# Kernel tuning notes

Measured on AMD Instinct MI355X. Metric: run time of the kernel, lower is better.

The kernel has to match this reference:

```python
import jax, jax.numpy as jnp
import numpy as np

FEAT_STRIDE = 16
PRE_NMS = 6000
POST_NMS = 300
NMS_THRESH = 0.7
NEG_THR = 0.3
POS_THR = 0.7
RPN_BATCH = 256
FG_FRAC = 0.5
SCALES = (8, 16, 32)
RATIOS = (0.5, 1.0, 2.0)
A = len(SCALES) * len(RATIOS)  # 9


def _generate_anchors():
    base = 16.0
    ctr = (base - 1.0) * 0.5
    size = base * base
    out = []
    for r in RATIOS:
        ws = np.round(np.sqrt(size / r))
        hs = np.round(ws * r)
        for s in SCALES:
            W = ws * s
            H = hs * s
            out.append([ctr - 0.5 * (W - 1), ctr - 0.5 * (H - 1),
                        ctr + 0.5 * (W - 1), ctr + 0.5 * (H - 1)])
    return np.array(out, np.float32)  # [9,4]


def _conv(x, w, b, pad):
    y = jax.lax.conv_general_dilated(x, w, (1, 1), [(pad, pad), (pad, pad)],
                                     dimension_numbers=('NCHW', 'OIHW', 'NCHW'))
    return y + b[None, :, None, None]


def _all_anchors(H, W):
    base = jnp.asarray(_generate_anchors())
    sx = jnp.arange(W, dtype=jnp.float32) * FEAT_STRIDE
    sy = jnp.arange(H, dtype=jnp.float32) * FEAT_STRIDE
    gy, gx = jnp.meshgrid(sy, sx, indexing='ij')
    shifts = jnp.stack([gx, gy, gx, gy], -1).reshape(-1, 1, 4)  # [H*W,1,4]
    return (shifts + base[None]).reshape(-1, 4)  # (h,w,a) order, [H*W*A,4]


def _decode(anchors, deltas):
    w = anchors[:, 2] - anchors[:, 0] + 1.0
    h = anchors[:, 3] - anchors[:, 1] + 1.0
    cx = anchors[:, 0] + 0.5 * w
    cy = anchors[:, 1] + 0.5 * h
    pcx = deltas[:, 0] * w + cx
    pcy = deltas[:, 1] * h + cy
    pw = jnp.exp(deltas[:, 2]) * w
    ph = jnp.exp(deltas[:, 3]) * h
    return jnp.stack([pcx - 0.5 * pw, pcy - 0.5 * ph, pcx + 0.5 * pw, pcy + 0.5 * ph], -1)


def _encode(anchors, gt):
    ew = anchors[:, 2] - anchors[:, 0] + 1.0
    eh = anchors[:, 3] - anchors[:, 1] + 1.0
    ecx = anchors[:, 0] + 0.5 * ew
    ecy = anchors[:, 1] + 0.5 * eh
    gw = gt[:, 2] - gt[:, 0] + 1.0
    gh = gt[:, 3] - gt[:, 1] + 1.0
    gcx = gt[:, 0] + 0.5 * gw
    gcy = gt[:, 1] + 0.5 * gh
    return jnp.stack([(gcx - ecx) / ew, (gcy - ecy) / eh,
                      jnp.log(gw / ew), jnp.log(gh / eh)], -1)


def _nms(boxes, scores, thresh, max_out):
    x1, y1, x2, y2 = boxes[:, 0], boxes[:, 1], boxes[:, 2], boxes[:, 3]
    areas = (x2 - x1 + 1.0) * (y2 - y1 + 1.0)
    N = boxes.shape[0]

    def body(k, st):
        valid, sel, selv = st
        s = jnp.where(valid, scores, -jnp.inf)
        i = jnp.argmax(s)
        ok = s[i] > -jnp.inf
        iw = jnp.maximum(jnp.minimum(x2[i], x2) - jnp.maximum(x1[i], x1) + 1.0, 0.0)
        ih = jnp.maximum(jnp.minimum(y2[i], y2) - jnp.maximum(y1[i], y1) + 1.0, 0.0)
        inter = iw * ih
        iou = inter / (areas[i] + areas - inter)
        valid = valid & (iou <= thresh)
        return valid, sel.at[k].set(i.astype(jnp.int32)), selv.at[k].set(ok)

    st = jax.lax.fori_loop(0, max_out, body,
                           (jnp.ones(N, bool), jnp.zeros(max_out, jnp.int32), jnp.zeros(max_out, bool)))
    return st[1], st[2]


def _propose_one(scores, deltas, anchors, imh, imw):
    boxes = _decode(anchors, deltas)
    boxes = jnp.stack([jnp.clip(boxes[:, 0], 0.0, imw - 1.0),
                       jnp.clip(boxes[:, 1], 0.0, imh - 1.0),
                       jnp.clip(boxes[:, 2], 0.0, imw - 1.0),
                       jnp.clip(boxes[:, 3], 0.0, imh - 1.0)], -1)
    top_s, idx = jax.lax.top_k(scores, PRE_NMS)
    top_b = boxes[idx]
    sel, selv = _nms(top_b, top_s, NMS_THRESH, POST_NMS)
    return top_b[sel] * selv[:, None].astype(top_b.dtype)  # [POST_NMS,4], zero rows when exhausted


def _anchor_target_one(gt, imh, imw, rfg, rbg, anchors):
    N = anchors.shape[0]
    ax1, ay1, ax2, ay2 = anchors[:, 0], anchors[:, 1], anchors[:, 2], anchors[:, 3]
    inside = (ax1 >= 0) & (ay1 >= 0) & (ax2 < imw) & (ay2 < imh)
    gx1, gy1, gx2, gy2 = gt[:, 0], gt[:, 1], gt[:, 2], gt[:, 3]
    gw = gx2 - gx1 + 1.0
    gh = gy2 - gy1 + 1.0
    gt_valid = ~((gw == 1.0) & (gh == 1.0))  # all-zero padded gt boxes
    aw = ax2 - ax1 + 1.0
    ah = ay2 - ay1 + 1.0
    iw = jnp.maximum(jnp.minimum(ax2[:, None], gx2[None, :]) - jnp.maximum(ax1[:, None], gx1[None, :]) + 1.0, 0.0)
    ih = jnp.maximum(jnp.minimum(ay2[:, None], gy2[None, :]) - jnp.maximum(ay1[:, None], gy1[None, :]) + 1.0, 0.0)
    inter = iw * ih
    iou = inter / ((aw * ah)[:, None] + (gw * gh)[None, :] - inter)  # [N,K]
    iou = jnp.where(gt_valid[None, :], iou, 0.0)
    iou = jnp.where(inside[:, None], iou, -1.0)  # outside anchors excluded, as in original
    max_ov = iou.max(1)
    arg = iou.argmax(1)
    gt_max = iou.max(0)
    gt_max = jnp.where(gt_max <= 0.0, 1e-5, gt_max)
    keep = (iou == gt_max[None, :]).any(1)  # anchors with max overlap per gt -> fg
    labels = jnp.full(N, -1.0, jnp.float32)
    labels = jnp.where(max_ov < NEG_THR, 0.0, labels)
    labels = jnp.where(keep, 1.0, labels)
    labels = jnp.where(max_ov >= POS_THR, 1.0, labels)
    labels = jnp.where(inside, labels, -1.0)

    def ranks(r, mask):
        order = jnp.argsort(jnp.where(mask, r, 2.0))
        return jnp.zeros(N, jnp.int32).at[order].set(jnp.arange(N, dtype=jnp.int32))

    num_fg = int(FG_FRAC * RPN_BATCH)
    fg_keep = (labels == 1.0) & (ranks(rfg, labels == 1.0) < num_fg)
    num_bg = RPN_BATCH - fg_keep.sum()
    bg_keep = (labels == 0.0) & (ranks(rbg, labels == 0.0) < num_bg)
    labels = jnp.where(fg_keep, 1.0, jnp.where(bg_keep, 0.0, -1.0))
    targets = _encode(anchors, gt[arg, :4])
    ones4 = jnp.ones((1, 4), jnp.float32)
    in_w = (labels == 1.0).astype(jnp.float32)[:, None] * ones4
    n_ex = (labels >= 0).sum().astype(jnp.float32)
    out_w = jnp.where(labels >= 0, 1.0 / n_ex, 0.0)[:, None] * ones4
    return labels, targets, in_w, out_w


def _rpn_forward(base_feat, im_info, gt_boxes, conv_w, conv_b, cls_w, cls_b, bbox_w, bbox_b):
    B, _, H, W = base_feat.shape
    x = jax.nn.relu(_conv(base_feat, conv_w, conv_b, 1))
    cls_score = _conv(x, cls_w, cls_b, 0)                 # [B,2A,H,W]
    # reshape(x,2) -> softmax over axis 1 -> reshape back
    prob = jax.nn.softmax(cls_score.reshape(B, 2, A * H, W), axis=1).reshape(B, 2 * A, H, W)
    bbox_pred = _conv(x, bbox_w, bbox_b, 0)               # [B,4A,H,W]
    anchors = _all_anchors(H, W)                          # [H*W*A,4]

    # ---- proposal layer (detached in original) ----
    fg = prob[:, A:, :, :].transpose(0, 2, 3, 1).reshape(B, -1)        # (h,w,a)
    deltas = bbox_pred.transpose(0, 2, 3, 1).reshape(B, -1, 4)
    rois_boxes = jax.vmap(_propose_one, in_axes=(0, 0, None, 0, 0))(
        jax.lax.stop_gradient(fg), jax.lax.stop_gradient(deltas), anchors, im_info[:, 0], im_info[:, 1])
    batch_idx = jnp.broadcast_to(jnp.arange(B, dtype=rois_boxes.dtype)[:, None, None], (B, POST_NMS, 1))
    rois = jnp.concatenate([batch_idx, rois_boxes], -1)   # [B,POST_NMS,5]

    # ---- anchor target layer (training path) ----
    key = jax.random.key(42)
    rfg = jax.random.uniform(key, (B, anchors.shape[0]))
    rbg = jax.random.uniform(jax.random.fold_in(key, 1), (B, anchors.shape[0]))
    labels, targets, in_w, out_w = jax.vmap(_anchor_target_one, in_axes=(0, 0, 0, 0, 0, None))(
        gt_boxes, im_info[:, 0], im_info[:, 1], rfg, rbg, anchors)
    # rearrange (h,w,a) -> (a,h,w) layouts to match torch permutes
    labels = labels.reshape(B, H, W, A).transpose(0, 3, 1, 2).reshape(B, -1)
    targets = targets.reshape(B, H, W, A * 4).transpose(0, 3, 1, 2)
    in_w = in_w.reshape(B, H, W, A * 4).transpose(0, 3, 1, 2)
    out_w = out_w.reshape(B, H, W, A * 4).transpose(0, 3, 1, 2)

    # cross-entropy over kept anchors
    logits = cls_score.reshape(B, 2, A, H, W).transpose(0, 2, 3, 4, 1).reshape(-1, 2)
    lab = labels.reshape(-1)
    m = (lab >= 0).astype(logits.dtype)
    logp = jax.nn.log_softmax(logits, axis=-1)
    idx = jnp.clip(lab, 0.0, 1.0).astype(jnp.int32)
    nll = -jnp.take_along_axis(logp, idx[:, None], axis=1)[:, 0]
    loss_cls = (nll * m).sum() / m.sum()

    # smooth-L1 box loss, sigma=3, sum dims [1,2,3] then mean over batch
    sigma2 = 9.0
    diff = in_w * (bbox_pred - targets)
    ad = jnp.abs(diff)
    flag = (ad < 1.0 / sigma2).astype(diff.dtype)
    lb = flag * 0.5 * sigma2 * diff * diff + (1.0 - flag) * (ad - 0.5 / sigma2)
    loss_box = (out_w * lb).sum(axis=(1, 2, 3)).mean()
    return rois, loss_cls, loss_box


def setup_inputs() -> dict:
    key = jax.random.key(0)
    ks = jax.random.split(key, 9)
    B, C, H, W = 4, 512, 50, 76
    base_feat = jax.random.normal(ks[0], (B, C, H, W), jnp.float32)
    conv_w = jax.random.normal(ks[1], (512, C, 3, 3), jnp.float32) * 0.01
    conv_b = jnp.zeros((512,), jnp.float32)
    cls_w = jax.random.normal(ks[2], (18, 512, 1, 1), jnp.float32) * 0.01
    cls_b = jnp.zeros((18,), jnp.float32)
    bbox_w = jax.random.normal(ks[3], (36, 512, 1, 1), jnp.float32) * 0.01
    bbox_b = jnp.zeros((36,), jnp.float32)
    imh, imw = float(H * FEAT_STRIDE), float(W * FEAT_STRIDE)
    im_info = jnp.tile(jnp.array([imh, imw, 1.0], jnp.float32), (B, 1))
    K = 20
    cx = jax.random.uniform(ks[4], (B, K)) * (imw - 100.0) + 50.0
    cy = jax.random.uniform(ks[5], (B, K)) * (imh - 100.0) + 50.0
    bw = jax.random.uniform(ks[6], (B, K)) * 270.0 + 30.0
    bh = jax.random.uniform(ks[7], (B, K)) * 270.0 + 30.0
    x1 = jnp.clip(cx - 0.5 * bw, 0.0, imw - 1.0)
    x2 = jnp.clip(cx + 0.5 * bw, 0.0, imw - 1.0)
    y1 = jnp.clip(cy - 0.5 * bh, 0.0, imh - 1.0)
    y2 = jnp.clip(cy + 0.5 * bh, 0.0, imh - 1.0)
    cls = jax.random.randint(ks[8], (B, K), 1, 21).astype(jnp.float32)
    gt_boxes = jnp.stack([x1, y1, x2, y2, cls], -1)
    num_boxes = jnp.full((B,), K, jnp.int32)
    return {"base_feat": base_feat, "im_info": im_info, "gt_boxes": gt_boxes,
            "num_boxes": num_boxes, "conv_w": conv_w, "conv_b": conv_b,
            "cls_w": cls_w, "cls_b": cls_b, "bbox_w": bbox_w, "bbox_b": bbox_b}


def reference(base_feat, im_info, gt_boxes, num_boxes, conv_w, conv_b, cls_w, cls_b, bbox_w, bbox_b):
    # num_boxes is implicitly handled via zero-padded gt_boxes (as in the original layer)
    return _rpn_forward(base_feat, im_info, gt_boxes, conv_w, conv_b, cls_w, cls_b, bbox_w, bbox_b)
```

## Files before the change

kernel.cpp:

```cpp
#include <hip/hip_runtime.h>
#include <stdint.h>

#define HHH 50
#define WWW 76
#define NPIX 3800
#define NA 34200
#define PRE 6000
#define POST 300
#define NW 94
#define CIN 512
#define COUT 512
#define NBATCH 4
#define NGT 20
#define TFHALF 68400u
#define XTB 2252800

typedef __bf16 bf16x8 __attribute__((ext_vector_type(8)));
typedef float f32x4 __attribute__((ext_vector_type(4)));
typedef unsigned int u32x4v __attribute__((ext_vector_type(4)));

__device__ static inline f32x4 MFMA16(bf16x8 a, bf16x8 b, f32x4 c) {
  return __builtin_amdgcn_mfma_f32_16x16x32_bf16(a, b, c, 0, 0, 0);
}
__device__ static inline bf16x8 LD8(const unsigned short* p) {
  return __builtin_bit_cast(bf16x8, *(const u32x4v*)p);
}

__host__ __device__ static inline void tf2x32(unsigned k0, unsigned k1, unsigned& x0, unsigned& x1) {
  unsigned k2 = k0 ^ k1 ^ 0x1BD11BDAu;
#define TFR(r) do { x0 += x1; x1 = (x1 << (r)) | (x1 >> (32 - (r))); x1 ^= x0; } while (0)
  x0 += k0; x1 += k1;
  TFR(13); TFR(15); TFR(26); TFR(6);
  x0 += k1; x1 += k2 + 1u;
  TFR(17); TFR(29); TFR(16); TFR(24);
  x0 += k2; x1 += k0 + 2u;
  TFR(13); TFR(15); TFR(26); TFR(6);
  x0 += k0; x1 += k1 + 3u;
  TFR(17); TFR(29); TFR(16); TFR(24);
  x0 += k1; x1 += k2 + 4u;
  TFR(13); TFR(15); TFR(26); TFR(6);
  x0 += k2; x1 += k0 + 5u;
#undef TFR
}

__device__ static inline unsigned tf_u23(unsigned k0, unsigned k1, unsigned p) {
  unsigned x0, x1;
  if (p < TFHALF) { x0 = p; x1 = p + TFHALF; tf2x32(k0, k1, x0, x1); return x0 >> 9; }
  x0 = p - TFHALF; x1 = p; tf2x32(k0, k1, x0, x1); return x1 >> 9;
}

__device__ const float BA[9][4] = {
  {-84.f, -40.f,  99.f,  55.f}, {-176.f, -88.f, 191.f, 103.f}, {-360.f, -184.f, 375.f, 199.f},
  {-56.f, -56.f,  71.f,  71.f}, {-120.f, -120.f, 135.f, 135.f}, {-248.f, -248.f, 263.f, 263.f},
  {-36.f, -80.f,  51.f,  95.f}, {-80.f, -168.f,  95.f, 183.f}, {-168.f, -344.f, 183.f, 359.f}
};

__device__ static inline unsigned monoF(float f) {
  int b = __float_as_int(f);
  unsigned u = (unsigned)b;
  return (b < 0) ? ~u : (u | 0x80000000u);
}
__device__ static inline float unmonoF(unsigned u) {
  unsigned b = (u & 0x80000000u) ? (u ^ 0x80000000u) : ~u;
  return __int_as_float((int)b);
}

__device__ static inline void split3(float v, unsigned short& h, unsigned short& m, unsigned short& l) {
  __bf16 b0 = (__bf16)v;  float f0 = (float)b0;
  float r = v - f0;       __bf16 b1 = (__bf16)r;  float f1 = (float)b1;
  float r2 = r - f1;      __bf16 b2 = (__bf16)r2;
  h = __builtin_bit_cast(unsigned short, b0);
  m = __builtin_bit_cast(unsigned short, b1);
  l = __builtin_bit_cast(unsigned short, b2);
}

__global__ void k_split_x(const float* __restrict__ feat, unsigned short* __restrict__ x0,
                          unsigned short* __restrict__ x1, unsigned short* __restrict__ x2) {
  int tid = blockIdx.x * 256 + threadIdx.x;
  if (tid >= NBATCH * XTB) return;
  int b = tid / XTB;
  int rem = tid - b * XTB;
  int pg = rem >> 13;
  int r2 = rem & 8191;
  int cg = r2 >> 7;
  int po = (r2 >> 3) & 15;
  int cl = r2 & 7;
  int ci = cg * 8 + cl;
  int px = pg * 16 + po;
  int hq = px / 80, wq = px - hq * 80;
  float v = 0.f;
  if (hq >= 2 && hq < 52 && wq >= 1 && wq < 77)
    v = feat[((size_t)(b * 512 + ci)) * NPIX + (hq - 2) * 76 + (wq - 1)];
  unsigned short h, m, l;
  split3(v, h, m, l);
  x0[tid] = h; x1[tid] = m; x2[tid] = l;
}

__global__ void k_split_w(const float* __restrict__ cw, unsigned short* __restrict__ w0,
                          unsigned short* __restrict__ w1, unsigned short* __restrict__ w2,
                          unsigned* __restrict__ gtmaxU, int* __restrict__ cnts, float* __restrict__ accums) {
  int tid = blockIdx.x * 256 + threadIdx.x;
  if (blockIdx.x == 0) {
    int t = threadIdx.x;
    if (t < NBATCH * NGT) gtmaxU[t] = 0x407FFFFFu;
    if (t < 8) cnts[t] = 0;
    if (t < 8) accums[t] = 0.f;
  }
  if (tid >= 9 * 64 * 512 * 8) return;
  int cl = tid & 7;
  int co = (tid >> 3) & 511;
  int cg = (tid >> 12) & 63;
  int tap = tid >> 18;
  int ci = cg * 8 + cl;
  float v = cw[((size_t)co * 512 + ci) * 9 + tap];
  unsigned short h, m, l;
  split3(v, h, m, l);
  w0[tid] = h; w1[tid] = m; w2[tid] = l;
}

__global__ void k_tr_w1(const float* __restrict__ clsw, const float* __restrict__ bbw, float* __restrict__ wt1) {
  int tid = blockIdx.x * 256 + threadIdx.x;
  if (tid >= CIN * 64) return;
  int c = tid & 63, ci = tid >> 6;
  float v = 0.f;
  if (c < 18) v = clsw[c * 512 + ci];
  else if (c < 54) v = bbw[(c - 18) * 512 + ci];
  wt1[tid] = v;
}

__global__ __launch_bounds__(256, 2) void k_conv3(
    const unsigned short* __restrict__ XT0, const unsigned short* __restrict__ XT1,
    const unsigned short* __restrict__ XT2,
    const unsigned short* __restrict__ WT0, const unsigned short* __restrict__ WT1,
    const unsigned short* __restrict__ WT2,
    const float* __restrict__ bias, float* __restrict__ out) {
  const int d = blockIdx.x;
  const int copair = (d >> 1) & 3, half = d & 1, g = d >> 3;
  const int cob = copair * 2 + (g & 1);
  const int pxb = half * 64 + (g >> 1);
  const int pxp = pxb & 31, b = pxb >> 5;
  const int co0 = cob * 64;
  const int px0 = 160 + pxp * 128;
  const int t = threadIdx.x, l = t & 63, wv = t >> 6;
  const int wr = wv >> 1, wc = wv & 1;
  const int l15 = l & 15, lq = l >> 4;
  f32x4 cmain[2][4], ccorr[2][4];
  double accd[2][4][4];
#pragma unroll
  for (int c = 0; c < 2; ++c)
#pragma unroll
    for (int p = 0; p < 4; ++p) {
      cmain[c][p] = (f32x4)(0.f); ccorr[c][p] = (f32x4)(0.f);
#pragma unroll
      for (int r = 0; r < 4; ++r) accd[c][p][r] = 0.0;
    }
  const unsigned short* xt0 = XT0 + (size_t)b * XTB;
  const unsigned short* xt1 = XT1 + (size_t)b * XTB;
  const unsigned short* xt2 = XT2 + (size_t)b * XTB;
  const int coA = wr * 32 + l15;
  const int OFFT[9] = {-81, -80, -79, -1, 0, 1, 79, 80, 81};
  const int pxw = px0 + wc * 64 + l15;

  for (int kg = 0; kg < 16; ++kg) {
    const int cgl = kg * 4 + lq;
    const int cglo = cgl * 128;
    const size_t aro = ((size_t)cgl * 512 + co0 + coA) * 8;
#pragma unroll
    for (int tap = 0; tap < 9; ++tap) {
      const size_t ao = aro + (size_t)tap * (64 * 512 * 8);
      bf16x8 A0[2], A1[2], A2[2];
      A0[0] = LD8(WT0 + ao); A0[1] = LD8(WT0 + ao + 128);
      A1[0] = LD8(WT1 + ao); A1[1] = LD8(WT1 + ao + 128);
      A2[0] = LD8(WT2 + ao); A2[1] = LD8(WT2 + ao + 128);
      const int pxbase = pxw + OFFT[tap];
      const size_t eob = (size_t)((pxbase >> 4) * 8192 + (pxbase & 15) * 8 + cglo);
#pragma unroll
      for (int p = 0; p < 4; ++p) {
        const size_t eo = eob + (size_t)p * 8192;
        bf16x8 B0 = LD8(xt0 + eo);
        bf16x8 B1 = LD8(xt1 + eo);
        bf16x8 B2 = LD8(xt2 + eo);
#pragma unroll
        for (int c = 0; c < 2; ++c) {
          cmain[c][p] = MFMA16(A0[c], B0, cmain[c][p]);
          ccorr[c][p] = MFMA16(A2[c], B0, ccorr[c][p]);
          ccorr[c][p] = MFMA16(A0[c], B2, ccorr[c][p]);
          ccorr[c][p] = MFMA16(A1[c], B1, ccorr[c][p]);
          ccorr[c][p] = MFMA16(A1[c], B0, ccorr[c][p]);
          ccorr[c][p] = MFMA16(A0[c], B1, ccorr[c][p]);
        }
      }
    }
    if (kg & 1) {
#pragma unroll
      for (int c = 0; c < 2; ++c)
#pragma unroll
        for (int p = 0; p < 4; ++p) {
#pragma unroll
          for (int r = 0; r < 4; ++r) accd[c][p][r] += (double)cmain[c][p][r];
          cmain[c][p] = (f32x4)(0.f);
        }
    }
  }
  const size_t outb = ((size_t)b * 512 + co0) * NPIX;
#pragma unroll
  for (int c = 0; c < 2; ++c)
#pragma unroll
    for (int p = 0; p < 4; ++p)
#pragma unroll
      for (int r = 0; r < 4; ++r) {
        int coL = wr * 32 + c * 16 + lq * 4 + r;
        int px = px0 + wc * 64 + p * 16 + l15;
        int hq = px / 80, wq = px - hq * 80;
        if (hq >= 2 && hq < 52 && wq >= 1 && wq < 77) {
          float v = (float)(accd[c][p][r] + (double)ccorr[c][p][r]) + bias[co0 + coL];
          out[outb + (size_t)coL * NPIX + (hq - 2) * 76 + (wq - 1)] = fmaxf(v, 0.f);
        }
      }
}

__global__ __launch_bounds__(256) void k_conv1(const float* __restrict__ x, const float* __restrict__ wt1,
                                               const float* __restrict__ clsb, const float* __restrict__ bbb,
                                               float* __restrict__ clsS, float* __restrict__ bbp) {
  const int b = blockIdx.y;
  const int px0 = blockIdx.x * 128;
  const int t = threadIdx.x;
  const int cg = t & 7, pg = t >> 3;
  __shared__ float xs[16][128];
  __shared__ float ws[16][72];
  double acc[8][4];
#pragma unroll
  for (int i = 0; i < 8; ++i)
#pragma unroll
    for (int j = 0; j < 4; ++j) acc[i][j] = 0.0;
  const float* xb = x + (size_t)b * CIN * NPIX;
  for (int cc = 0; cc < CIN; cc += 16) {
#pragma unroll
    for (int e0 = 0; e0 < 8; ++e0) {
      int e = t + e0 * 256;
      int r = e >> 7, c = e & 127;
      int p = px0 + c;
      xs[r][c] = (p < NPIX) ? xb[(size_t)(cc + r) * NPIX + p] : 0.f;
    }
#pragma unroll
    for (int e0 = 0; e0 < 4; ++e0) {
      int e = t + e0 * 256;
      int r = e >> 6, c = e & 63;
      ws[r][c + ((c >> 5) << 2)] = wt1[(cc + r) * 64 + c];
    }
    __syncthreads();
    const int wcol = (cg << 3) + ((cg >> 2) << 2);
    const int xcol = pg << 2;
    float a32[8][4];
#pragma unroll
    for (int i = 0; i < 8; ++i)
#pragma unroll
      for (int j = 0; j < 4; ++j) a32[i][j] = 0.f;
#pragma unroll
    for (int k = 0; k < 16; ++k) {
      const float4 w0 = *(const float4*)&ws[k][wcol];
      const float4 w1 = *(const float4*)&ws[k][wcol + 4];
      const float4 xa = *(const float4*)&xs[k][xcol];
      const float wv[8] = {w0.x, w0.y, w0.z, w0.w, w1.x, w1.y, w1.z, w1.w};
      const float xv[4] = {xa.x, xa.y, xa.z, xa.w};
#pragma unroll
      for (int i = 0; i < 8; ++i)
#pragma unroll
        for (int j = 0; j < 4; ++j)
          a32[i][j] = fmaf(wv[i], xv[j], a32[i][j]);
    }
#pragma unroll
    for (int i = 0; i < 8; ++i)
#pragma unroll
      for (int j = 0; j < 4; ++j) acc[i][j] += (double)a32[i][j];
    __syncthreads();
  }
#pragma unroll
  for (int i = 0; i < 8; ++i) {
    int c = cg * 8 + i;
#pragma unroll
    for (int j = 0; j < 4; ++j) {
      int p = px0 + pg * 4 + j;
      if (p < NPIX) {
        if (c < 18) clsS[((size_t)b * 18 + c) * NPIX + p] = (float)acc[i][j] + clsb[c];
        else if (c < 54) bbp[((size_t)b * 36 + (c - 18)) * NPIX + p] = (float)acc[i][j] + bbb[c - 18];
      }
    }
  }
}

__global__ void k_decode(const float* __restrict__ clsS, const float* __restrict__ bbp,
                         const float* __restrict__ im_info, float* __restrict__ boxes,
                         unsigned long long* __restrict__ keys) {
  int tid = blockIdx.x * 256 + threadIdx.x;
  if (tid >= NBATCH * NA) return;
  int b = tid / NA, n = tid - b * NA;
  int a = n % 9, p = n / 9;
  int h = p / WWW, w = p - h * WWW;
  const float* cb = clsS + (size_t)b * 18 * NPIX;
  float s0 = cb[(size_t)a * NPIX + p];
  float s1 = cb[(size_t)(9 + a) * NPIX + p];
  float mx = fmaxf(s0, s1);
  float e0 = expf(s0 - mx), e1 = expf(s1 - mx);
  float fg = e1 / (e0 + e1);
  const float* bb = bbp + (size_t)b * 36 * NPIX;
  float d0 = bb[(size_t)(a * 4 + 0) * NPIX + p];
  float d1 = bb[(size_t)(a * 4 + 1) * NPIX + p];
  float d2 = bb[(size_t)(a * 4 + 2) * NPIX + p];
  float d3 = bb[(size_t)(a * 4 + 3) * NPIX + p];
  float ax1 = BA[a][0] + w * 16.f, ay1 = BA[a][1] + h * 16.f;
  float ax2 = BA[a][2] + w * 16.f, ay2 = BA[a][3] + h * 16.f;
  float aw = ax2 - ax1 + 1.f, ah = ay2 - ay1 + 1.f;
  float acx = ax1 + 0.5f * aw, acy = ay1 + 0.5f * ah;
  float pcx = d0 * aw + acx, pcy = d1 * ah + acy;
  float pw = expf(d2) * aw, ph = expf(d3) * ah;
  float imh = im_info[b * 3 + 0], imw = im_info[b * 3 + 1];
  float x1 = fminf(fmaxf(pcx - 0.5f * pw, 0.f), imw - 1.f);
  float y1 = fminf(fmaxf(pcy - 0.5f * ph, 0.f), imh - 1.f);
  float x2 = fminf(fmaxf(pcx + 0.5f * pw, 0.f), imw - 1.f);
  float y2 = fminf(fmaxf(pcy + 0.5f * ph, 0.f), imh - 1.f);
  float* bx = boxes + ((size_t)b * NA + n) * 4;
  bx[0] = x1; bx[1] = y1; bx[2] = x2; bx[3] = y2;
  unsigned fb = __float_as_uint(fg);
  keys[((size_t)b << 16) + n] = ((unsigned long long)fb << 32) | (unsigned)(~(unsigned)n);
}

__global__ __launch_bounds__(1024) void k_rsel_top(const unsigned long long* __restrict__ keys,
                                                   unsigned long long* __restrict__ comp) {
  const int b = blockIdx.x;
  const unsigned long long* kb = keys + ((size_t)b << 16);
  __shared__ int hist[16][256];
  __shared__ int histT[256];
  __shared__ unsigned long long sh_prefix;
  __shared__ unsigned sh_r;
  __shared__ int sh_cnt;
  const int t = threadIdx.x, wid = t >> 6, lane = t & 63;
  if (t == 0) { sh_prefix = 0ull; sh_r = PRE; sh_cnt = 0; }
  __syncthreads();
  for (int p = 5; p >= 0; --p) {
    for (int e = t; e < 4096; e += 1024) ((int*)hist)[e] = 0;
    __syncthreads();
    unsigned long long pref = sh_prefix;
    for (int i = t; i < NA; i += 1024) {
      unsigned long long k = kb[i];
      unsigned long long k48 = ((k >> 16) & 0xFFFFFFFF0000ull) | (k & 0xFFFFull);
      bool m = (p == 5) || ((k48 >> (8 * (p + 1))) == pref);
      if (m) atomicAdd(&hist[wid][(int)((k48 >> (8 * p)) & 255)], 1);
    }
    __syncthreads();
    if (t < 256) { int s = 0; for (int w = 0; w < 16; ++w) s += hist[w][t]; histT[t] = s; }
    __syncthreads();
    if (t == 0) {
      unsigned rr = sh_r; unsigned cum = 0;
      for (int v = 255; v >= 0; --v) {
        cum += (unsigned)histT[v];
        if (cum >= rr) { sh_r = rr - (cum - (unsigned)histT[v]); sh_prefix = (sh_prefix << 8) | (unsigned)v; break; }
      }
    }
    __syncthreads();
  }
  const unsigned long long thr48 = sh_prefix;
  for (int base = 0; base < NA; base += 1024) {
    int i = base + t;
    bool keep = false;
    unsigned long long k = 0ull;
    if (i < NA) {
      k = kb[i];
      unsigned long long k48 = ((k >> 16) & 0xFFFFFFFF0000ull) | (k & 0xFFFFull);
      keep = (k48 >= thr48);
    }
    unsigned long long bal = __ballot(keep);
    if (bal) {
      int leader = __ffsll(bal) - 1;
      int basepos = 0;
      if (lane == leader) basepos = atomicAdd(&sh_cnt, (int)__popcll(bal));
      basepos = __shfl(basepos, leader);
      if (keep) {
        int off = __popcll(bal & ((1ull << lane) - 1ull));
        comp[b * 8192 + basepos + off] = k;
      }
    }
  }
}

__global__ __launch_bounds__(1024) void k_sort_lds(const unsigned long long* __restrict__ comp,
                                                   const float* __restrict__ boxes,
                                                   float* __restrict__ tbx1, float* __restrict__ tby1,
                                                   float* __restrict__ tbx2, float* __restrict__ tby2,
                                                   float* __restrict__ tba) {
  __shared__ unsigned long long s[8192];
  const int b = blockIdx.x;
  const int t = threadIdx.x;
  const unsigned long long* cb = comp + b * 8192;
  for (int e = t; e < 8192; e += 1024) s[e] = (e < PRE) ? cb[e] : 0ull;
  __syncthreads();
  for (int k = 2; k <= 8192; k <<= 1) {
    for (int j = k >> 1; j >= 1; j >>= 1) {
      for (int q = t; q < 4096; q += 1024) {
        int i = ((q & ~(j - 1)) << 1) | (q & (j - 1));
        int pp = i | j;
        bool up = (i & k) == 0;
        unsigned long long a = s[i], d = s[pp];
        if (up ? (a < d) : (a > d)) { s[i] = d; s[pp] = a; }
      }
      __syncthreads();
    }
  }
  for (int e = t; e < PRE; e += 1024) {
    unsigned long long key = s[e];
    unsigned n = ~(unsigned)(key & 0xFFFFFFFFu);
    const float* bx = boxes + ((size_t)b * NA + n) * 4;
    float x1 = bx[0], y1 = bx[1], x2 = bx[2], y2 = bx[3];
    int o = b * PRE + e;
    tbx1[o] = x1; tby1[o] = y1; tbx2[o] = x2; tby2[o] = y2;
    tba[o] = (x2 - x1 + 1.f) * (y2 - y1 + 1.f);
  }
}

__global__ __launch_bounds__(256) void k_mask(const float* __restrict__ tbx1, const float* __restrict__ tby1,
                                              const float* __restrict__ tbx2, const float* __restrict__ tby2,
                                              const float* __restrict__ tba, unsigned long long* __restrict__ mask) {
  const int b = blockIdx.y;
  const int i0 = blockIdx.x * 64;
  const int t = threadIdx.x;
  __shared__ float jx1[2048], jy1[2048], jx2[2048], jy2[2048], ja[2048];
  __shared__ float ix1[64], iy1[64], ix2[64], iy2[64], ia[64];
  const float* bx1 = tbx1 + b * PRE;
  const float* by1 = tby1 + b * PRE;
  const float* bx2 = tbx2 + b * PRE;
  const float* by2 = tby2 + b * PRE;
  const float* ba2 = tba + b * PRE;
  if (t < 64) {
    int i = i0 + t;
    if (i < PRE) { ix1[t] = bx1[i]; iy1[t] = by1[i]; ix2[t] = bx2[i]; iy2[t] = by2[i]; ia[t] = ba2[i]; }
    else { ix1[t] = 0; iy1[t] = 0; ix2[t] = 0; iy2[t] = 0; ia[t] = 1; }
  }
  for (int c = 0; c < 3; ++c) {
    int j0 = c * 2048;
    for (int e = t; e < 2048; e += 256) {
      int j = j0 + e;
      if (j < PRE) { jx1[e] = bx1[j]; jy1[e] = by1[j]; jx2[e] = bx2[j]; jy2[e] = by2[j]; ja[e] = ba2[j]; }
      else { jx1[e] = 0; jy1[e] = 0; jx2[e] = 0; jy2[e] = 0; ja[e] = 1; }
    }
    __syncthreads();
    for (int task = t; task < 64 * 32; task += 256) {
      int il = task & 63, wl = task >> 6;
      int i = i0 + il;
      int wg = (j0 >> 6) + wl;
      if (i >= PRE || wg >= NW) continue;
      unsigned long long word = 0ull;
      float X1 = ix1[il], Y1 = iy1[il], X2 = ix2[il], Y2 = iy2[il], A = ia[il];
      for (int l = 0; l < 64; ++l) {
        int j = wg * 64 + l;
        if (j > i && j < PRE) {
          int e = j - j0;
          float iw = fminf(X2, jx2[e]) - fmaxf(X1, jx1[e]) + 1.f;
          float ih = fminf(Y2, jy2[e]) - fmaxf(Y1, jy1[e]) + 1.f;
          if (iw > 0.f && ih > 0.f) {
            float inter = iw * ih;
            float iou = inter / (A + ja[e] - inter);
            if (iou > 0.7f) word |= (1ull << l);
          }
        }
      }
      mask[((size_t)(b * PRE + i)) * NW + wg] = word;
    }
    __syncthreads();
  }
}

__global__ void k_nms(const unsigned long long* __restrict__ mask,
                      const float* __restrict__ tbx1, const float* __restrict__ tby1,
                      const float* __restrict__ tbx2, const float* __restrict__ tby2,
                      float* __restrict__ out) {
  const int b = blockIdx.x;
  const int lane = threadIdx.x;
  unsigned long long rem0 = 0ull;
  unsigned long long rem1;
  if (64 + lane < NW) rem1 = (64 + lane == NW - 1) ? ~((1ull << (PRE - (NW - 1) * 64)) - 1ull) : 0ull;
  else rem1 = ~0ull;
  int sc = 0;
  for (; sc < POST; ++sc) {
    unsigned long long a0 = ~rem0, a1 = ~rem1;
    unsigned long long bal0 = __ballot(a0 != 0ull);
    int w, l;
    if (bal0) {
      int src = __ffsll(bal0) - 1;
      unsigned long long av = __shfl(a0, src);
      w = src; l = __ffsll(av) - 1;
    } else {
      unsigned long long bal1 = __ballot(a1 != 0ull);
      if (!bal1) break;
      int src = __ffsll(bal1) - 1;
      unsigned long long av = __shfl(a1, src);
      w = 64 + src; l = __ffsll(av) - 1;
    }
    int j = w * 64 + l;
    if (lane < 5) {
      float v;
      if (lane == 0) v = (float)b;
      else if (lane == 1) v = tbx1[b * PRE + j];
      else if (lane == 2) v = tby1[b * PRE + j];
      else if (lane == 3) v = tbx2[b * PRE + j];
      else v = tby2[b * PRE + j];
      out[((size_t)(b * POST + sc)) * 5 + lane] = v;
    }
    const unsigned long long* row = mask + ((size_t)(b * PRE + j)) * NW;
    rem0 |= row[lane];
    if (64 + lane < NW) rem1 |= row[64 + lane];
    if (w < 64) { if (lane == w) rem0 |= (1ull << l); }
    else if (lane == w - 64) rem1 |= (1ull << l);
  }
  for (int r2 = sc; r2 < POST; ++r2)
    if (lane < 5) out[((size_t)(b * POST + r2)) * 5 + lane] = (lane == 0) ? (float)b : 0.f;
}

__global__ __launch_bounds__(256) void k_iouA(const float* __restrict__ gt_boxes, const float* __restrict__ im_info,
                                              float* __restrict__ iou, float* __restrict__ maxov,
                                              int* __restrict__ argm, unsigned* __restrict__ gtmaxU) {
  const int b = blockIdx.y;
  const int n = blockIdx.x * 256 + threadIdx.x;
  const int t = threadIdx.x, lane = t & 63, wv = t >> 6;
  __shared__ float g[NGT][6];
  __shared__ float wmax[4][NGT];
  if (t < NGT) {
    const float* gg = gt_boxes + (b * NGT + t) * 5;
    float x1 = gg[0], y1 = gg[1], x2 = gg[2], y2 = gg[3];
    g[t][0] = x1; g[t][1] = y1; g[t][2] = x2; g[t][3] = y2;
    float gw = x2 - x1 + 1.f, gh = y2 - y1 + 1.f;
    g[t][4] = gw * gh;
    g[t][5] = ((gw == 1.f) && (gh == 1.f)) ? 0.f : 1.f;
  }
  __syncthreads();
  const bool act = (n < NA);
  float vj[NGT];
  float best = -2.f;
  int barg = 0;
  if (act) {
    int a = n % 9, p = n / 9;
    int h = p / WWW, w = p - h * WWW;
    float ax1 = BA[a][0] + w * 16.f, ay1 = BA[a][1] + h * 16.f;
    float ax2 = BA[a][2] + w * 16.f, ay2 = BA[a][3] + h * 16.f;
    float imh = im_info[b * 3 + 0], imw = im_info[b * 3 + 1];
    bool inside = (ax1 >= 0.f) && (ay1 >= 0.f) && (ax2 < imw) && (ay2 < imh);
    float aw = ax2 - ax1 + 1.f, ah = ay2 - ay1 + 1.f;
    float aa = aw * ah;
    float* row = iou + ((size_t)(b * NA) + n) * NGT;
#pragma unroll
    for (int j = 0; j < NGT; ++j) {
      float iw = fmaxf(fminf(ax2, g[j][2]) - fmaxf(ax1, g[j][0]) + 1.f, 0.f);
      float ih = fmaxf(fminf(ay2, g[j][3]) - fmaxf(ay1, g[j][1]) + 1.f, 0.f);
      float inter = iw * ih;
      float v = inter / (aa + g[j][4] - inter);
      if (g[j][5] == 0.f) v = 0.f;
      if (!inside) v = -1.f;
      row[j] = v;
      vj[j] = v;
      if (v > best) { best = v; barg = j; }
    }
    maxov[b * NA + n] = best;
    argm[b * NA + n] = barg;
  } else {
#pragma unroll
    for (int j = 0; j < NGT; ++j) vj[j] = -1.f;
  }
#pragma unroll
  for (int j = 0; j < NGT; ++j) {
    float red = vj[j];
    for (int o = 32; o > 0; o >>= 1) red = fmaxf(red, __shfl_xor(red, o));
    if (lane == 0) wmax[wv][j] = red;
  }
  __syncthreads();
  if (t < NGT) {
    float m = fmaxf(fmaxf(wmax[0][t], wmax[1][t]), fmaxf(wmax[2][t], wmax[3][t]));
    if (m > 0.f) atomicMax(&gtmaxU[b * NGT + t], monoF(m));
  }
}

__global__ __launch_bounds__(256) void k_labels(const float* __restrict__ iou, const float* __restrict__ maxov,
                                                const unsigned* __restrict__ gtmaxU, const float* __restrict__ im_info,
                                                unsigned kf0, unsigned kf1, unsigned kb0, unsigned kb1,
                                                int* __restrict__ labels, unsigned* __restrict__ ufg,
                                                unsigned* __restrict__ ubg, int* __restrict__ cnts) {
  const int b = blockIdx.y;
  const int n = blockIdx.x * 256 + threadIdx.x;
  __shared__ float gmf[NGT];
  if (threadIdx.x < NGT) {
    float gm = unmonoF(gtmaxU[b * NGT + threadIdx.x]);
    gmf[threadIdx.x] = (gm <= 0.f) ? 1e-5f : gm;
  }
  __syncthreads();
  int label = -1;
  if (n < NA) {
    int a = n % 9, p = n / 9;
    int h = p / WWW, w = p - h * WWW;
    float ax1 = BA[a][0] + w * 16.f, ay1 = BA[a][1] + h * 16.f;
    float ax2 = BA[a][2] + w * 16.f, ay2 = BA[a][3] + h * 16.f;
    float imh = im_info[b * 3 + 0], imw = im_info[b * 3 + 1];
    bool inside = (ax1 >= 0.f) && (ay1 >= 0.f) && (ax2 < imw) && (ay2 < imh);
    float mo = maxov[b * NA + n];
    const float* row = iou + ((size_t)(b * NA) + n) * NGT;
    bool keep = false;
#pragma unroll
    for (int j = 0; j < NGT; ++j) keep = keep || (row[j] == gmf[j]);
    if (mo < 0.3f) label = 0;
    if (keep) label = 1;
    if (mo >= 0.7f) label = 1;
    if (!inside) label = -1;
    labels[b * NA + n] = label;
    unsigned pp = (unsigned)(b * NA + n);
    ufg[b * NA + n] = (label == 1) ? tf_u23(kf0, kf1, pp) : 0x00FFFFFFu;
    ubg[b * NA + n] = (label == 0) ? tf_u23(kb0, kb1, pp) : 0x00FFFFFFu;
  }
  unsigned long long bf = __ballot(label == 1);
  unsigned long long bb = __ballot(label == 0);
  if ((threadIdx.x & 63) == 0) {
    atomicAdd(&cnts[b], (int)__popcll(bf));
    atomicAdd(&cnts[4 + b], (int)__popcll(bb));
  }
}

__global__ __launch_bounds__(1024) void k_rsel_samp(const unsigned* __restrict__ ufg, const unsigned* __restrict__ ubg,
                                                    const int* __restrict__ cnts, unsigned* __restrict__ selp,
                                                    float* __restrict__ nexf) {
  const int blk = blockIdx.x;
  const int b = blk >> 1, cls = blk & 1;
  const unsigned* u = (cls == 0 ? ufg : ubg) + (size_t)b * NA;
  const int fcnt = cnts[b], bcnt = cnts[4 + b];
  const int kk = (cls == 0) ? 128 : (256 - (fcnt < 128 ? fcnt : 128));
  const int cnt = (cls == 0) ? fcnt : bcnt;
  const int t = threadIdx.x, wid = t >> 6;
  __shared__ int hist[16][256];
  __shared__ int histT[256];
  __shared__ unsigned long long sh_prefix;
  __shared__ unsigned sh_r;
  if (t == 0) {
    if (cls == 1) {
      int fk = fcnt < 128 ? fcnt : 128;
      int bk2 = bcnt < kk ? bcnt : kk;
      nexf[b] = (float)(fk + bk2);
    }
    sh_prefix = 0ull; sh_r = (unsigned)kk;
  }
  __syncthreads();
  if (kk > cnt) {
    if (t == 0) { selp[blk * 2] = 0x00FFFFFFu; selp[blk * 2 + 1] = 0x1FFFFu; }
    return;
  }
  for (int p = 4; p >= 0; --p) {
    for (int e = t; e < 4096; e += 1024) ((int*)hist)[e] = 0;
    __syncthreads();
    unsigned long long pref = sh_prefix;
    for (int i = t; i < NA; i += 1024) {
      unsigned uv = u[i];
      if (uv == 0x00FFFFFFu) continue;
      unsigned long long k = ((unsigned long long)uv << 17) | (unsigned)i;
      if ((k >> (8 * (p + 1))) == pref)
        atomicAdd(&hist[wid][(int)((k >> (8 * p)) & 255)], 1);
    }
    __syncthreads();
    if (t < 256) { int s = 0; for (int w = 0; w < 16; ++w) s += hist[w][t]; histT[t] = s; }
    __syncthreads();
    if (t == 0) {
      unsigned rr = sh_r; unsigned cum = 0;
      for (int v = 0; v < 256; ++v) {
        cum += (unsigned)histT[v];
        if (cum >= rr) { sh_r = rr - (cum - (unsigned)histT[v]); sh_prefix = (sh_prefix << 8) | (unsigned)v; break; }
      }
    }
    __syncthreads();
  }
  if (t == 0) {
    selp[blk * 2] = (unsigned)(sh_prefix >> 17);
    selp[blk * 2 + 1] = (unsigned)(sh_prefix & 0x1FFFF);
  }
}

__global__ __launch_bounds__(256) void k_loss(const float* __restrict__ clsS, const float* __restrict__ bbp,
                                              const float* __restrict__ gt_boxes, const int* __restrict__ labels,
                                              const unsigned* __restrict__ ufg, const unsigned* __restrict__ ubg,
                                              const unsigned* __restrict__ selp, const int* __restrict__ argm,
                                              float* __restrict__ accums) {
  const int b = blockIdx.y;
  const int n = blockIdx.x * 256 + threadIdx.x;
  float nll = 0.f, mcnt = 0.f, lbsum = 0.f;
  if (n < NA) {
    int label = labels[b * NA + n];
    int fin = -1;
    if (label == 1) {
      unsigned uu = ufg[b * NA + n];
      unsigned thr = selp[(b * 2 + 0) * 2], ithr = selp[(b * 2 + 0) * 2 + 1];
      if (uu < thr || (uu == thr && (unsigned)n <= ithr)) fin = 1;
    } else if (label == 0) {
      unsigned uu = ubg[b * NA + n];
      unsigned thr = selp[(b * 2 + 1) * 2], ithr = selp[(b * 2 + 1) * 2 + 1];
      if (uu < thr || (uu == thr && (unsigned)n <= ithr)) fin = 0;
    }
    if (fin >= 0) {
      int a = n % 9, p = n / 9;
      float s0 = clsS[((size_t)b * 18 + a) * NPIX + p];
      float s1 = clsS[((size_t)b * 18 + 9 + a) * NPIX + p];
      float mx = fmaxf(s0, s1);
      float lse = mx + logf(expf(s0 - mx) + expf(s1 - mx));
      nll = lse - (fin == 1 ? s1 : s0);
      mcnt = 1.f;
      if (fin == 1) {
        int h = p / WWW, w = p - h * WWW;
        float ax1 = BA[a][0] + w * 16.f, ay1 = BA[a][1] + h * 16.f;
        float ax2 = BA[a][2] + w * 16.f, ay2 = BA[a][3] + h * 16.f;
        float ew = ax2 - ax1 + 1.f, eh = ay2 - ay1 + 1.f;
        float ecx = ax1 + 0.5f * ew, ecy = ay1 + 0.5f * eh;
        int ag = argm[b * NA + n];
        const float* gg = gt_boxes + (b * NGT + ag) * 5;
        float gw = gg[2] - gg[0] + 1.f, gh = gg[3] - gg[1] + 1.f;
        float gcx = gg[0] + 0.5f * gw, gcy = gg[1] + 0.5f * gh;
        float tt[4];
        tt[0] = (gcx - ecx) / ew;
        tt[1] = (gcy - ecy) / eh;
        tt[2] = logf(gw / ew);
        tt[3] = logf(gh / eh);
#pragma unroll
        for (int dd = 0; dd < 4; ++dd) {
          float pd = bbp[((size_t)b * 36 + (a * 4 + dd)) * NPIX + p];
          float diff = pd - tt[dd];
          float ad = fabsf(diff);
          lbsum += (ad < 1.f / 9.f) ? 4.5f * diff * diff : (ad - 0.5f / 9.f);
        }
      }
    }
  }
  for (int o = 32; o > 0; o >>= 1) {
    nll += __shfl_down(nll, o);
    mcnt += __shfl_down(mcnt, o);
    lbsum += __shfl_down(lbsum, o);
  }
  __shared__ float p0[4], p1[4], p2[4];
  int wid = threadIdx.x >> 6;
  if ((threadIdx.x & 63) == 0) { p0[wid] = nll; p1[wid] = mcnt; p2[wid] = lbsum; }
  __syncthreads();
  if (threadIdx.x == 0) {
    float aS = 0, bS = 0, cS = 0;
    for (int q = 0; q < 4; ++q) { aS += p0[q]; bS += p1[q]; cS += p2[q]; }
    atomicAdd(&accums[0], aS);
    atomicAdd(&accums[1], bS);
    atomicAdd(&accums[2 + b], cS);
  }
}

__global__ void k_final(const float* __restrict__ accums, const float* __restrict__ nexf, float* __restrict__ out) {
  if (threadIdx.x == 0 && blockIdx.x == 0) {
    out[6000] = accums[0] / accums[1];
    float lb = 0.f;
    for (int b = 0; b < NBATCH; ++b) lb += accums[2 + b] / nexf[b];
    out[6001] = lb * 0.25f;
  }
}

extern "C" void kernel_launch(void* const* d_in, const int* in_sizes, int n_in,
                              void* d_out, int out_size, void* d_ws, size_t ws_size,
                              hipStream_t stream) {
  (void)in_sizes; (void)n_in; (void)out_size; (void)ws_size;
  const float* base_feat = (const float*)d_in[0];
  const float* im_info   = (const float*)d_in[1];
  const float* gt_boxes  = (const float*)d_in[2];
  const float* conv_w    = (const float*)d_in[4];
  const float* conv_b    = (const float*)d_in[5];
  const float* cls_w     = (const float*)d_in[6];
  const float* cls_b     = (const float*)d_in[7];
  const float* bbox_w    = (const float*)d_in[8];
  const float* bbox_b    = (const float*)d_in[9];
  float* out = (float*)d_out;

  char* wp = (char*)d_ws;
  auto carve = [&](size_t bytes) -> void* {
    void* r = (void*)wp;
    wp += (bytes + 255) & ~(size_t)255;
    return r;
  };
  float* x     = (float*)carve((size_t)NBATCH * CIN * NPIX * 4);
  float* clsS  = (float*)carve((size_t)NBATCH * 18 * NPIX * 4);
  float* bbp   = (float*)carve((size_t)NBATCH * 36 * NPIX * 4);
  unsigned short* WT0 = (unsigned short*)carve((size_t)9 * 64 * 512 * 8 * 2);
  unsigned short* WT1 = (unsigned short*)carve((size_t)9 * 64 * 512 * 8 * 2);
  unsigned short* WT2 = (unsigned short*)carve((size_t)9 * 64 * 512 * 8 * 2);
  float* wt1   = (float*)carve((size_t)CIN * 64 * 4);
  unsigned* gtmaxU = (unsigned*)carve(NBATCH * NGT * 4);
  int* cnts    = (int*)carve(8 * 4);
  unsigned* selp = (unsigned*)carve(16 * 4);
  float* nexf  = (float*)carve(4 * 4);
  float* accums = (float*)carve(8 * 4);

  char* overlay = wp;
  unsigned short* XT0 = (unsigned short*)overlay;
  unsigned short* XT1 = XT0 + (size_t)NBATCH * XTB;
  unsigned short* XT2 = XT1 + (size_t)NBATCH * XTB;
  char* wp2 = overlay;
  auto carve2 = [&](size_t bytes) -> void* {
    void* r = (void*)wp2;
    wp2 += (bytes + 255) & ~(size_t)255;
    return r;
  };
  float* boxes = (float*)carve2((size_t)NBATCH * NA * 4 * 4);
  unsigned long long* keys = (unsigned long long*)carve2((size_t)NBATCH * 65536 * 8);
  float* tbx1 = (float*)carve2((size_t)NBATCH * PRE * 4);
  float* tby1 = (float*)carve2((size_t)NBATCH * PRE * 4);
  float* tbx2 = (float*)carve2((size_t)NBATCH * PRE * 4);
  float* tby2 = (float*)carve2((size_t)NBATCH * PRE * 4);
  float* tba  = (float*)carve2((size_t)NBATCH * PRE * 4);
  unsigned long long* mask = (unsigned long long*)carve2((size_t)NBATCH * PRE * NW * 8);
  float* iou   = (float*)carve2((size_t)NBATCH * NA * NGT * 4);
  float* maxov = (float*)carve2((size_t)NBATCH * NA * 4);
  int* argm    = (int*)carve2((size_t)NBATCH * NA * 4);
  int* labels  = (int*)carve2((size_t)NBATCH * NA * 4);
  unsigned* ufg = (unsigned*)carve2((size_t)NBATCH * NA * 4);
  unsigned* ubg = (unsigned*)carve2((size_t)NBATCH * NA * 4);
  unsigned long long* comp = (unsigned long long*)carve2((size_t)NBATCH * 8192 * 8);

  unsigned kb0 = 0u, kb1 = 1u;
  tf2x32(0u, 42u, kb0, kb1);

  k_split_w<<<dim3((9 * 64 * 512 * 8) / 256), dim3(256), 0, stream>>>(conv_w, WT0, WT1, WT2, gtmaxU, cnts, accums);
  k_tr_w1<<<dim3((CIN * 64) / 256), dim3(256), 0, stream>>>(cls_w, bbox_w, wt1);
  k_split_x<<<dim3((NBATCH * XTB + 255) / 256), dim3(256), 0, stream>>>(base_feat, XT0, XT1, XT2);
  k_conv3<<<dim3(1024), dim3(256), 0, stream>>>(XT0, XT1, XT2, WT0, WT1, WT2, conv_b, x);
  k_conv1<<<dim3(30, 4), dim3(256), 0, stream>>>(x, wt1, cls_b, bbox_b, clsS, bbp);
  k_decode<<<dim3((NBATCH * NA + 255) / 256), dim3(256), 0, stream>>>(clsS, bbp, im_info, boxes, keys);
  k_rsel_top<<<dim3(NBATCH), dim3(1024), 0, stream>>>(keys, comp);
  k_sort_lds<<<dim3(NBATCH), dim3(1024), 0, stream>>>(comp, boxes, tbx1, tby1, tbx2, tby2, tba);
  k_mask<<<dim3(NW, NBATCH), dim3(256), 0, stream>>>(tbx1, tby1, tbx2, tby2, tba, mask);
  k_nms<<<dim3(NBATCH), dim3(64), 0, stream>>>(mask, tbx1, tby1, tbx2, tby2, out);
  k_iouA<<<dim3((NA + 255) / 256, NBATCH), dim3(256), 0, stream>>>(gt_boxes, im_info, iou, maxov, argm, gtmaxU);
  k_labels<<<dim3((NA + 255) / 256, NBATCH), dim3(256), 0, stream>>>(iou, maxov, gtmaxU, im_info,
                                                                     0u, 42u, kb0, kb1, labels, ufg, ubg, cnts);
  k_rsel_samp<<<dim3(8), dim3(1024), 0, stream>>>(ufg, ubg, cnts, selp, nexf);
  k_loss<<<dim3((NA + 255) / 256, NBATCH), dim3(256), 0, stream>>>(clsS, bbp, gt_boxes, labels, ufg, ubg, selp, argm, accums);
  k_final<<<dim3(1), dim3(1), 0, stream>>>(accums, nexf, out);
}
```

Baseline: 1.430 ms.

## Stage split_x through LDS, skip lower-triangle NMS mask, recompute anchor IoU

k_split_x now runs one block per channel group and batch. It loads 8 channels into a padded LDS tile with coalesced reads, then writes the bf16 split layout, replacing strided per-element gathers from global memory. k_mask skips IoU work for mask words that lie entirely below the diagonal and just writes zeros. The IoU matrix and maxov buffers are removed: k_labels recomputes IoU against the GT boxes itself and computes argmax, trading some recomputation for less global memory traffic. The LDS tile uses about 140KB per block, which limits occupancy.

```diff
diff --git a/kernel.cpp b/kernel.cpp
--- a/kernel.cpp
+++ b/kernel.cpp
@@ -74,26 +74,38 @@
   l = __builtin_bit_cast(unsigned short, b2);
 }
 
-__global__ void k_split_x(const float* __restrict__ feat, unsigned short* __restrict__ x0,
-                          unsigned short* __restrict__ x1, unsigned short* __restrict__ x2) {
-  int tid = blockIdx.x * 256 + threadIdx.x;
-  if (tid >= NBATCH * XTB) return;
-  int b = tid / XTB;
-  int rem = tid - b * XTB;
-  int pg = rem >> 13;
-  int r2 = rem & 8191;
-  int cg = r2 >> 7;
-  int po = (r2 >> 3) & 15;
-  int cl = r2 & 7;
-  int ci = cg * 8 + cl;
-  int px = pg * 16 + po;
-  int hq = px / 80, wq = px - hq * 80;
-  float v = 0.f;
-  if (hq >= 2 && hq < 52 && wq >= 1 && wq < 77)
-    v = feat[((size_t)(b * 512 + ci)) * NPIX + (hq - 2) * 76 + (wq - 1)];
-  unsigned short h, m, l;
-  split3(v, h, m, l);
-  x0[tid] = h; x1[tid] = m; x2[tid] = l;
+__global__ __launch_bounds__(256) void k_split_x(const float* __restrict__ feat,
+                                                 unsigned short* __restrict__ x0,
+                                                 unsigned short* __restrict__ x1,
+                                                 unsigned short* __restrict__ x2) {
+  __shared__ float ldsb[8 * 4401];
+  const int cg = blockIdx.x, b = blockIdx.y;
+  const int t = threadIdx.x;
+  for (int e = t; e < 8 * 4401; e += 256) ldsb[e] = 0.f;
+  __syncthreads();
+  const float* fb = feat + ((size_t)(b * 512 + cg * 8)) * NPIX;
+#pragma unroll
+  for (int r = 0; r < 8; ++r) {
+    for (int i = t; i < NPIX; i += 256) {
+      int h = i / 76, w = i - h * 76;
+      ldsb[r * 4401 + (h + 2) * 80 + w + 1] = fb[(size_t)r * NPIX + i];
+    }
+  }
+  __syncthreads();
+  const size_t obase = (size_t)b * XTB + (size_t)cg * 128;
+  for (int pgb = 0; pgb < 276; pgb += 2) {
+    int pg = pgb + (t >> 7);
+    int e = t & 127;
+    if (pg < 275) {
+      int po = e >> 3, cl = e & 7;
+      int px = pg * 16 + po;
+      float v = ldsb[cl * 4401 + px];
+      unsigned short hh, mm, ll;
+      split3(v, hh, mm, ll);
+      size_t o = obase + (size_t)pg * 8192 + e;
+      x0[o] = hh; x1[o] = mm; x2[o] = ll;
+    }
+  }
 }
 
 __global__ void k_split_w(const float* __restrict__ cw, unsigned short* __restrict__ w0,
@@ -421,7 +433,8 @@
                                               const float* __restrict__ tbx2, const float* __restrict__ tby2,
                                               const float* __restrict__ tba, unsigned long long* __restrict__ mask) {
   const int b = blockIdx.y;
-  const int i0 = blockIdx.x * 64;
+  const int iblk = blockIdx.x;
+  const int i0 = iblk * 64;
   const int t = threadIdx.x;
   __shared__ float jx1[2048], jy1[2048], jx2[2048], jy2[2048], ja[2048];
   __shared__ float ix1[64], iy1[64], ix2[64], iy2[64], ia[64];
@@ -437,6 +450,15 @@
   }
   for (int c = 0; c < 3; ++c) {
     int j0 = c * 2048;
+    if (c * 32 + 31 < iblk) {
+      for (int task = t; task < 64 * 32; task += 256) {
+        int il = task & 63, wl = task >> 6;
+        int i = i0 + il;
+        int wg = c * 32 + wl;
+        if (i < PRE && wg < NW) mask[((size_t)(b * PRE + i)) * NW + wg] = 0ull;
+      }
+      continue;
+    }
     for (int e = t; e < 2048; e += 256) {
       int j = j0 + e;
       if (j < PRE) { jx1[e] = bx1[j]; jy1[e] = by1[j]; jx2[e] = bx2[j]; jy2[e] = by2[j]; ja[e] = ba2[j]; }
@@ -446,8 +468,9 @@
     for (int task = t; task < 64 * 32; task += 256) {
       int il = task & 63, wl = task >> 6;
       int i = i0 + il;
-      int wg = (j0 >> 6) + wl;
+      int wg = c * 32 + wl;
       if (i >= PRE || wg >= NW) continue;
+      if (wg < iblk) { mask[((size_t)(b * PRE + i)) * NW + wg] = 0ull; continue; }
       unsigned long long word = 0ull;
       float X1 = ix1[il], Y1 = iy1[il], X2 = ix2[il], Y2 = iy2[il], A = ia[il];
       for (int l = 0; l < 64; ++l) {
@@ -515,9 +538,8 @@
     if (lane < 5) out[((size_t)(b * POST + r2)) * 5 + lane] = (lane == 0) ? (float)b : 0.f;
 }
 
-__global__ __launch_bounds__(256) void k_iouA(const float* __restrict__ gt_boxes, const float* __restrict__ im_info,
-                                              float* __restrict__ iou, float* __restrict__ maxov,
-                                              int* __restrict__ argm, unsigned* __restrict__ gtmaxU) {
+__global__ __launch_bounds__(256) void k_gtmax(const float* __restrict__ gt_boxes, const float* __restrict__ im_info,
+                                               unsigned* __restrict__ gtmaxU) {
   const int b = blockIdx.y;
   const int n = blockIdx.x * 256 + threadIdx.x;
   const int t = threadIdx.x, lane = t & 63, wv = t >> 6;
@@ -532,11 +554,8 @@
     g[t][5] = ((gw == 1.f) && (gh == 1.f)) ? 0.f : 1.f;
   }
   __syncthreads();
-  const bool act = (n < NA);
   float vj[NGT];
-  float best = -2.f;
-  int barg = 0;
-  if (act) {
+  if (n < NA) {
     int a = n % 9, p = n / 9;
     int h = p / WWW, w = p - h * WWW;
     float ax1 = BA[a][0] + w * 16.f, ay1 = BA[a][1] + h * 16.f;
@@ -545,7 +564,6 @@
     bool inside = (ax1 >= 0.f) && (ay1 >= 0.f) && (ax2 < imw) && (ay2 < imh);
     float aw = ax2 - ax1 + 1.f, ah = ay2 - ay1 + 1.f;
     float aa = aw * ah;
-    float* row = iou + ((size_t)(b * NA) + n) * NGT;
 #pragma unroll
     for (int j = 0; j < NGT; ++j) {
       float iw = fmaxf(fminf(ax2, g[j][2]) - fmaxf(ax1, g[j][0]) + 1.f, 0.f);
@@ -554,12 +572,8 @@
       float v = inter / (aa + g[j][4] - inter);
       if (g[j][5] == 0.f) v = 0.f;
       if (!inside) v = -1.f;
-      row[j] = v;
       vj[j] = v;
-      if (v > best) { best = v; barg = j; }
-    }
-    maxov[b * NA + n] = best;
-    argm[b * NA + n] = barg;
+    }
   } else {
 #pragma unroll
     for (int j = 0; j < NGT; ++j) vj[j] = -1.f;
@@ -577,17 +591,26 @@
   }
 }
 
-__global__ __launch_bounds__(256) void k_labels(const float* __restrict__ iou, const float* __restrict__ maxov,
+__global__ __launch_bounds__(256) void k_labels(const float* __restrict__ gt_boxes,
                                                 const unsigned* __restrict__ gtmaxU, const float* __restrict__ im_info,
                                                 unsigned kf0, unsigned kf1, unsigned kb0, unsigned kb1,
                                                 int* __restrict__ labels, unsigned* __restrict__ ufg,
-                                                unsigned* __restrict__ ubg, int* __restrict__ cnts) {
+                                                unsigned* __restrict__ ubg, int* __restrict__ cnts,
+                                                int* __restrict__ argm) {
   const int b = blockIdx.y;
   const int n = blockIdx.x * 256 + threadIdx.x;
+  const int t = threadIdx.x;
+  __shared__ float g[NGT][6];
   __shared__ float gmf[NGT];
-  if (threadIdx.x < NGT) {
-    float gm = unmonoF(gtmaxU[b * NGT + threadIdx.x]);
-    gmf[threadIdx.x] = (gm <= 0.f) ? 1e-5f : gm;
+  if (t < NGT) {
+    const float* gg = gt_boxes + (b * NGT + t) * 5;
+    float x1 = gg[0], y1 = gg[1], x2 = gg[2], y2 = gg[3];
+    g[t][0] = x1; g[t][1] = y1; g[t][2] = x2; g[t][3] = y2;
+    float gw = x2 - x1 + 1.f, gh = y2 - y1 + 1.f;
+    g[t][4] = gw * gh;
+    g[t][5] = ((gw == 1.f) && (gh == 1.f)) ? 0.f : 1.f;
+    float gm = unmonoF(gtmaxU[b * NGT + t]);
+    gmf[t] = (gm <= 0.f) ? 1e-5f : gm;
   }
   __syncthreads();
   int label = -1;
@@ -598,16 +621,29 @@
     float ax2 = BA[a][2] + w * 16.f, ay2 = BA[a][3] + h * 16.f;
     float imh = im_info[b * 3 + 0], imw = im_info[b * 3 + 1];
     bool inside = (ax1 >= 0.f) && (ay1 >= 0.f) && (ax2 < imw) && (ay2 < imh);
-    float mo = maxov[b * NA + n];
-    const float* row = iou + ((size_t)(b * NA) + n) * NGT;
+    float aw = ax2 - ax1 + 1.f, ah = ay2 - ay1 + 1.f;
+    float aa = aw * ah;
+    float best = -2.f;
+    int barg = 0;
     bool keep = false;
 #pragma unroll
-    for (int j = 0; j < NGT; ++j) keep = keep || (row[j] == gmf[j]);
+    for (int j = 0; j < NGT; ++j) {
+      float iw = fmaxf(fminf(ax2, g[j][2]) - fmaxf(ax1, g[j][0]) + 1.f, 0.f);
+      float ih = fmaxf(fminf(ay2, g[j][3]) - fmaxf(ay1, g[j][1]) + 1.f, 0.f);
+      float inter = iw * ih;
+      float v = inter / (aa + g[j][4] - inter);
+      if (g[j][5] == 0.f) v = 0.f;
+      if (!inside) v = -1.f;
+      keep = keep || (v == gmf[j]);
+      if (v > best) { best = v; barg = j; }
+    }
+    float mo = best;
     if (mo < 0.3f) label = 0;
     if (keep) label = 1;
     if (mo >= 0.7f) label = 1;
     if (!inside) label = -1;
     labels[b * NA + n] = label;
+    argm[b * NA + n] = barg;
     unsigned pp = (unsigned)(b * NA + n);
     ufg[b * NA + n] = (label == 1) ? tf_u23(kf0, kf1, pp) : 0x00FFFFFFu;
     ubg[b * NA + n] = (label == 0) ? tf_u23(kb0, kb1, pp) : 0x00FFFFFFu;
@@ -808,8 +844,6 @@
   float* tby2 = (float*)carve2((size_t)NBATCH * PRE * 4);
   float* tba  = (float*)carve2((size_t)NBATCH * PRE * 4);
   unsigned long long* mask = (unsigned long long*)carve2((size_t)NBATCH * PRE * NW * 8);
-  float* iou   = (float*)carve2((size_t)NBATCH * NA * NGT * 4);
-  float* maxov = (float*)carve2((size_t)NBATCH * NA * 4);
   int* argm    = (int*)carve2((size_t)NBATCH * NA * 4);
   int* labels  = (int*)carve2((size_t)NBATCH * NA * 4);
   unsigned* ufg = (unsigned*)carve2((size_t)NBATCH * NA * 4);
@@ -821,7 +855,7 @@
 
   k_split_w<<<dim3((9 * 64 * 512 * 8) / 256), dim3(256), 0, stream>>>(conv_w, WT0, WT1, WT2, gtmaxU, cnts, accums);
   k_tr_w1<<<dim3((CIN * 64) / 256), dim3(256), 0, stream>>>(cls_w, bbox_w, wt1);
-  k_split_x<<<dim3((NBATCH * XTB + 255) / 256), dim3(256), 0, stream>>>(base_feat, XT0, XT1, XT2);
+  k_split_x<<<dim3(64, NBATCH), dim3(256), 0, stream>>>(base_feat, XT0, XT1, XT2);
   k_conv3<<<dim3(1024), dim3(256), 0, stream>>>(XT0, XT1, XT2, WT0, WT1, WT2, conv_b, x);
   k_conv1<<<dim3(30, 4), dim3(256), 0, stream>>>(x, wt1, cls_b, bbox_b, clsS, bbp);
   k_decode<<<dim3((NBATCH * NA + 255) / 256), dim3(256), 0, stream>>>(clsS, bbp, im_info, boxes, keys);
@@ -829,9 +863,9 @@
   k_sort_lds<<<dim3(NBATCH), dim3(1024), 0, stream>>>(comp, boxes, tbx1, tby1, tbx2, tby2, tba);
   k_mask<<<dim3(NW, NBATCH), dim3(256), 0, stream>>>(tbx1, tby1, tbx2, tby2, tba, mask);
   k_nms<<<dim3(NBATCH), dim3(64), 0, stream>>>(mask, tbx1, tby1, tbx2, tby2, out);
-  k_iouA<<<dim3((NA + 255) / 256, NBATCH), dim3(256), 0, stream>>>(gt_boxes, im_info, iou, maxov, argm, gtmaxU);
-  k_labels<<<dim3((NA + 255) / 256, NBATCH), dim3(256), 0, stream>>>(iou, maxov, gtmaxU, im_info,
-                                                                     0u, 42u, kb0, kb1, labels, ufg, ubg, cnts);
+  k_gtmax<<<dim3((NA + 255) / 256, NBATCH), dim3(256), 0, stream>>>(gt_boxes, im_info, gtmaxU);
+  k_labels<<<dim3((NA + 255) / 256, NBATCH), dim3(256), 0, stream>>>(gt_boxes, gtmaxU, im_info,
+                                                                     0u, 42u, kb0, kb1, labels, ufg, ubg, cnts, argm);
   k_rsel_samp<<<dim3(8), dim3(1024), 0, stream>>>(ufg, ubg, cnts, selp, nexf);
   k_loss<<<dim3((NA + 255) / 256, NBATCH), dim3(256), 0, stream>>>(clsS, bbp, gt_boxes, labels, ufg, ubg, selp, argm, accums);
   k_final<<<dim3(1), dim3(1), 0, stream>>>(accums, nexf, out);
```

Result: no change. 1.448 ms (+1.2%).
